# Optimization experiments

Measured on AMD Instinct MI355X. Metric: run time of the kernel, lower is better.

## Reference

```python
import jax, jax.numpy as jnp
import numpy as np

ALPHA = 0.1
EPS = 1e-10

def setup_inputs() -> dict:
    key = jax.random.key(0)
    k1, k2 = jax.random.split(key)
    x = jax.random.normal(k1, (64, 8192, 128), dtype=jnp.float32)   # [B, N, D]
    pv = jax.random.uniform(k2, (64, 128), dtype=jnp.float32)        # [M, D] prototypes (torch.rand init)
    return {"x": x, "pv": pv}

def _cdist(x, pv):
    # Euclidean pairwise distance via GEMM form: [B,N,D] x [M,D] -> [B,N,M]
    x2 = jnp.sum(x * x, axis=-1, keepdims=True)          # [B,N,1]
    p2 = jnp.sum(pv * pv, axis=-1)                        # [M]
    xp = jnp.einsum('bnd,md->bnm', x, pv)                 # [B,N,M]
    return jnp.sqrt(jnp.maximum(x2 + p2 - 2.0 * xp, 0.0))

def reference(x, pv):
    dist = _cdist(x, pv)                                  # [B,N,M]
    min_dist = jnp.min(dist, axis=1)                      # [B,M] closest patch per prototype
    min_pos = jnp.argmin(dist, axis=1)                    # [B,M]
    # pick, per batch, the patch position of the globally closest prototype (no-grad in original)
    idx = jnp.argmin(min_dist, axis=1)                    # [B]
    min_pos = min_pos[jnp.arange(min_pos.shape[0]), idx]  # [B]
    max_sim = jnp.exp(EPS - ALPHA * min_dist)             # [B,M]
    return (max_sim, min_pos)
```

## Files before the change

kernel.cpp:

```cpp
#include <hip/hip_runtime.h>
#include <cfloat>
#include <cmath>

#define B_ 64
#define N_ 8192
#define D_ 128
#define M_ 64
#define CROWS 64
#define NCHUNK 4
#define BROWS (CROWS*NCHUNK)
#define NBLK (N_/BROWS)
#define ALPHA_ 0.1f
#define EPS_ 1e-10f

typedef __attribute__((ext_vector_type(4))) float f32x4;
typedef __attribute__((ext_vector_type(8))) short bf16x8;
typedef __attribute__((ext_vector_type(4))) short s16x4;

__global__ __launch_bounds__(256, 3)
void protomin_mfma(const float* __restrict__ x, const float* __restrict__ pv,
                   float* __restrict__ wsv, int* __restrict__ wsa) {
    __shared__ short xhi[CROWS * D_];
    __shared__ short xlo[CROWS * D_];
    __shared__ float x2s[CROWS];
    __shared__ float redv[2][M_];
    __shared__ int   redp[2][M_];

    const int tid = threadIdx.x;
    const int w   = tid >> 6;
    const int l   = tid & 63;
    const int lm  = l & 15, lg = l >> 4;
    const int wr  = w & 1;
    const int wm  = w >> 1;
    const int bid = blockIdx.x;
    const int b   = bid >> 5;
    const int nbase = (bid & 31) * BROWS;

    const float* xblk = x + ((size_t)b * N_ + nbase) * D_;

    f32x4 nv[8];
    {
        const f32x4* src = (const f32x4*)xblk;
#pragma unroll
        for (int i = 0; i < 8; ++i) nv[i] = src[(w * 8 + i) * 64 + l];
    }

    bf16x8 Bh[2][4], Bl[2][4];
#pragma unroll
    for (int mti = 0; mti < 2; ++mti) {
#pragma unroll
        for (int kt = 0; kt < 4; ++kt) {
            const float* p = pv + (wm * 32 + mti * 16 + lm) * D_ + kt * 32 + lg * 8;
#pragma unroll
            for (int h = 0; h < 2; ++h) {
                f32x4 pq = *(const f32x4*)(p + 4 * h);
#pragma unroll
                for (int j = 0; j < 4; ++j) {
                    unsigned u = __float_as_uint(pq[j]);
                    float hf = __uint_as_float(u & 0xffff0000u);
                    Bh[mti][kt][4 * h + j] = (short)(u >> 16);
                    float rem = pq[j] - hf;
                    Bl[mti][kt][4 * h + j] = (short)(__float_as_uint(rem) >> 16);
                }
            }
        }
    }

    auto stage = [&]() {
#pragma unroll
        for (int i = 0; i < 8; ++i) {
            int seg = w * 8 + i;
            int row = seg * 2 + (l >> 5);
            int ks  = (l & 31) * 4;
            f32x4 v = nv[i];
            float s = v[0] * v[0];
            s = fmaf(v[1], v[1], s); s = fmaf(v[2], v[2], s); s = fmaf(v[3], v[3], s);
            s += __shfl_xor(s, 1);  s += __shfl_xor(s, 2);  s += __shfl_xor(s, 4);
            s += __shfl_xor(s, 8);  s += __shfl_xor(s, 16);
            if ((l & 31) == 0) x2s[row] = s;
            s16x4 hv, lv;
#pragma unroll
            for (int j = 0; j < 4; ++j) {
                unsigned u = __float_as_uint(v[j]);
                float hf = __uint_as_float(u & 0xffff0000u);
                hv[j] = (short)(u >> 16);
                float rem = v[j] - hf;
                lv[j] = (short)(__float_as_uint(rem) >> 16);
            }
            int sidx = row * D_ + (ks ^ ((row & 7) << 3));
            *(s16x4*)&xhi[sidx] = hv;
            *(s16x4*)&xlo[sidx] = lv;
        }
    };

    float bv[2]; int bp[2];
#pragma unroll
    for (int mti = 0; mti < 2; ++mti) { bv[mti] = FLT_MAX; bp[mti] = 0; }

    stage();
    __syncthreads();

    for (int c = 0; c < NCHUNK; ++c) {
        if (c + 1 < NCHUNK) {
            const f32x4* src = (const f32x4*)(xblk + (size_t)(c + 1) * CROWS * D_);
#pragma unroll
            for (int i = 0; i < 8; ++i) nv[i] = src[(w * 8 + i) * 64 + l];
        }

        f32x4 acc[2][2] = {};
#pragma unroll
        for (int kt = 0; kt < 4; ++kt) {
            bf16x8 ah[2], al[2];
#pragma unroll
            for (int rt = 0; rt < 2; ++rt) {
                int arow = wr * 32 + rt * 16 + lm;
                int koff = (kt * 32 + lg * 8) ^ ((arow & 7) << 3);
                ah[rt] = *(const bf16x8*)&xhi[arow * D_ + koff];
                al[rt] = *(const bf16x8*)&xlo[arow * D_ + koff];
            }
#pragma unroll
            for (int rt = 0; rt < 2; ++rt) {
#pragma unroll
                for (int mti = 0; mti < 2; ++mti) {
                    acc[rt][mti] = __builtin_amdgcn_mfma_f32_16x16x32_bf16(ah[rt], Bh[mti][kt], acc[rt][mti], 0, 0, 0);
                    acc[rt][mti] = __builtin_amdgcn_mfma_f32_16x16x32_bf16(al[rt], Bh[mti][kt], acc[rt][mti], 0, 0, 0);
                    acc[rt][mti] = __builtin_amdgcn_mfma_f32_16x16x32_bf16(ah[rt], Bl[mti][kt], acc[rt][mti], 0, 0, 0);
                }
            }
        }

#pragma unroll
        for (int rt = 0; rt < 2; ++rt) {
            const int rbase = wr * 32 + rt * 16 + lg * 4;
            float x2v[4];
#pragma unroll
            for (int r = 0; r < 4; ++r) x2v[r] = x2s[rbase + r];
            const int npos0 = nbase + c * CROWS + rbase;
#pragma unroll
            for (int mti = 0; mti < 2; ++mti) {
#pragma unroll
                for (int r = 0; r < 4; ++r) {
                    float cand = fmaf(-2.f, acc[rt][mti][r], x2v[r]);
                    if (cand < bv[mti]) { bv[mti] = cand; bp[mti] = npos0 + r; }
                }
            }
        }

        if (c + 1 < NCHUNK) {
            __syncthreads();
            stage();
            __syncthreads();
        }
    }

#pragma unroll
    for (int mti = 0; mti < 2; ++mti) {
        float v = bv[mti]; int p = bp[mti];
#pragma unroll
        for (int off = 16; off <= 32; off <<= 1) {
            float ov = __shfl_xor(v, off);
            int   op = __shfl_xor(p, off);
            if (ov < v || (ov == v && op < p)) { v = ov; p = op; }
        }
        if (l < 16) { redv[wr][wm * 32 + mti * 16 + l] = v;
                      redp[wr][wm * 32 + mti * 16 + l] = p; }
    }
    __syncthreads();

    if (tid < M_) {
        float v = redv[0][tid]; int p = redp[0][tid];
        float ov = redv[1][tid]; int op = redp[1][tid];
        if (ov < v || (ov == v && op < p)) { v = ov; p = op; }
        wsv[(size_t)bid * M_ + tid] = v;
        wsa[(size_t)bid * M_ + tid] = p;
    }
}

__global__ void finalize_kernel(const float* __restrict__ wsv,
                                const int* __restrict__ wsa,
                                const float* __restrict__ pv,
                                float* __restrict__ out) {
    const int b = blockIdx.x;
    const int m = threadIdx.x;

    float p2 = 0.f;
    const f32x4* pp = (const f32x4*)(pv + m * D_);
#pragma unroll 8
    for (int j = 0; j < 32; ++j) {
        f32x4 v = pp[j];
        p2 = fmaf(v[0], v[0], p2); p2 = fmaf(v[1], v[1], p2);
        p2 = fmaf(v[2], v[2], p2); p2 = fmaf(v[3], v[3], p2);
    }

    float v = FLT_MAX; int p = 0;
    for (int bc = 0; bc < NBLK; ++bc) {
        size_t idx = ((size_t)(b * NBLK + bc)) * M_ + m;
        float nv2 = wsv[idx]; int np = wsa[idx];
        if (nv2 < v || (nv2 == v && np < p)) { v = nv2; p = np; }
    }
    float dist = sqrtf(fmaxf(v + p2, 0.f));
    out[b * M_ + m] = expf(EPS_ - ALPHA_ * dist);

    __shared__ float sv[M_];
    __shared__ int   sa[M_];
    sv[m] = dist; sa[m] = p;
    __syncthreads();
    if (m == 0) {
        float best = FLT_MAX; int bpos = 0;
        for (int k = 0; k < M_; ++k)
            if (sv[k] < best) { best = sv[k]; bpos = sa[k]; }
        out[B_ * M_ + b] = (float)bpos;
    }
}

extern "C" void kernel_launch(void* const* d_in, const int* in_sizes, int n_in,
                              void* d_out, int out_size, void* d_ws, size_t ws_size,
                              hipStream_t stream) {
    const float* x  = (const float*)d_in[0];
    const float* pv = (const float*)d_in[1];
    float* out = (float*)d_out;

    float* wsv = (float*)d_ws;
    int*   wsa = (int*)((char*)d_ws + (size_t)B_ * NBLK * M_ * sizeof(float));

    hipLaunchKernelGGL(protomin_mfma, dim3(B_ * NBLK), dim3(256), 0, stream,
                       x, pv, wsv, wsa);
    hipLaunchKernelGGL(finalize_kernel, dim3(B_), dim3(M_), 0, stream,
                       wsv, wsa, pv, out);
}
```

Before: 378.5 us.

## Stream x tiles straight into a double-buffered LDS ring via global_load_lds

```diff
diff --git a/kernel.cpp b/kernel.cpp
--- a/kernel.cpp
+++ b/kernel.cpp
@@ -15,14 +15,15 @@
 
 typedef __attribute__((ext_vector_type(4))) float f32x4;
 typedef __attribute__((ext_vector_type(8))) short bf16x8;
-typedef __attribute__((ext_vector_type(4))) short s16x4;
-
-__global__ __launch_bounds__(256, 3)
+
+#define GLOAD_LDS16(gp, lp) __builtin_amdgcn_global_load_lds(              \
+    (const __attribute__((address_space(1))) void*)(gp),                   \
+    (__attribute__((address_space(3))) void*)(lp), 16, 0, 0)
+
+__global__ __launch_bounds__(256, 2)
 void protomin_mfma(const float* __restrict__ x, const float* __restrict__ pv,
                    float* __restrict__ wsv, int* __restrict__ wsa) {
-    __shared__ short xhi[CROWS * D_];
-    __shared__ short xlo[CROWS * D_];
-    __shared__ float x2s[CROWS];
+    __shared__ float ring[2][CROWS * D_];
     __shared__ float redv[2][M_];
     __shared__ int   redp[2][M_];
 
@@ -38,12 +39,16 @@
 
     const float* xblk = x + ((size_t)b * N_ + nbase) * D_;
 
-    f32x4 nv[8];
-    {
-        const f32x4* src = (const f32x4*)xblk;
-#pragma unroll
-        for (int i = 0; i < 8; ++i) nv[i] = src[(w * 8 + i) * 64 + l];
-    }
+    auto issue = [&](int buf, int c) {
+#pragma unroll
+        for (int i = 0; i < 8; ++i) {
+            int s    = w * 8 + i;
+            int row  = 2 * s + (l >> 5);
+            int gsl  = (l & 31) ^ (row & 7);
+            const float* gp = xblk + (size_t)c * CROWS * D_ + row * D_ + gsl * 4;
+            GLOAD_LDS16(gp, &ring[buf][s * 256]);
+        }
+    };
 
     bf16x8 Bh[2][4], Bl[2][4];
 #pragma unroll
@@ -66,57 +71,56 @@
         }
     }
 
-    auto stage = [&]() {
-#pragma unroll
-        for (int i = 0; i < 8; ++i) {
-            int seg = w * 8 + i;
-            int row = seg * 2 + (l >> 5);
-            int ks  = (l & 31) * 4;
-            f32x4 v = nv[i];
-            float s = v[0] * v[0];
-            s = fmaf(v[1], v[1], s); s = fmaf(v[2], v[2], s); s = fmaf(v[3], v[3], s);
-            s += __shfl_xor(s, 1);  s += __shfl_xor(s, 2);  s += __shfl_xor(s, 4);
-            s += __shfl_xor(s, 8);  s += __shfl_xor(s, 16);
-            if ((l & 31) == 0) x2s[row] = s;
-            s16x4 hv, lv;
-#pragma unroll
-            for (int j = 0; j < 4; ++j) {
-                unsigned u = __float_as_uint(v[j]);
-                float hf = __uint_as_float(u & 0xffff0000u);
-                hv[j] = (short)(u >> 16);
-                float rem = v[j] - hf;
-                lv[j] = (short)(__float_as_uint(rem) >> 16);
-            }
-            int sidx = row * D_ + (ks ^ ((row & 7) << 3));
-            *(s16x4*)&xhi[sidx] = hv;
-            *(s16x4*)&xlo[sidx] = lv;
-        }
-    };
-
     float bv[2]; int bp[2];
 #pragma unroll
     for (int mti = 0; mti < 2; ++mti) { bv[mti] = FLT_MAX; bp[mti] = 0; }
 
-    stage();
+    issue(0, 0);
+    issue(1, 1);
     __syncthreads();
 
+#pragma unroll
     for (int c = 0; c < NCHUNK; ++c) {
-        if (c + 1 < NCHUNK) {
-            const f32x4* src = (const f32x4*)(xblk + (size_t)(c + 1) * CROWS * D_);
-#pragma unroll
-            for (int i = 0; i < 8; ++i) nv[i] = src[(w * 8 + i) * 64 + l];
-        }
-
+        const int buf = c & 1;
         f32x4 acc[2][2] = {};
+        float x2p[2] = {0.f, 0.f};
+
 #pragma unroll
         for (int kt = 0; kt < 4; ++kt) {
             bf16x8 ah[2], al[2];
 #pragma unroll
             for (int rt = 0; rt < 2; ++rt) {
-                int arow = wr * 32 + rt * 16 + lm;
-                int koff = (kt * 32 + lg * 8) ^ ((arow & 7) << 3);
-                ah[rt] = *(const bf16x8*)&xhi[arow * D_ + koff];
-                al[rt] = *(const bf16x8*)&xlo[arow * D_ + koff];
+                const int row = wr * 32 + rt * 16 + lm;
+                const int rs  = row & 7;
+                const int j0  = kt * 8 + lg * 2;
+                const float* base = &ring[buf][row * D_];
+                f32x4 v0 = *(const f32x4*)(base + (((j0    ) ^ rs) << 2));
+                f32x4 v1 = *(const f32x4*)(base + (((j0 + 1) ^ rs) << 2));
+                x2p[rt] = fmaf(v0[0], v0[0], x2p[rt]);
+                x2p[rt] = fmaf(v0[1], v0[1], x2p[rt]);
+                x2p[rt] = fmaf(v0[2], v0[2], x2p[rt]);
+                x2p[rt] = fmaf(v0[3], v0[3], x2p[rt]);
+                x2p[rt] = fmaf(v1[0], v1[0], x2p[rt]);
+                x2p[rt] = fmaf(v1[1], v1[1], x2p[rt]);
+                x2p[rt] = fmaf(v1[2], v1[2], x2p[rt]);
+                x2p[rt] = fmaf(v1[3], v1[3], x2p[rt]);
+                union { bf16x8 v; unsigned u[4]; } AH, AL;
+#pragma unroll
+                for (int pq = 0; pq < 2; ++pq) {
+                    f32x4 vv = pq ? v1 : v0;
+#pragma unroll
+                    for (int e = 0; e < 2; ++e) {
+                        unsigned u0 = __float_as_uint(vv[2 * e]);
+                        unsigned u1 = __float_as_uint(vv[2 * e + 1]);
+                        unsigned h0 = u0 & 0xffff0000u, h1 = u1 & 0xffff0000u;
+                        AH.u[pq * 2 + e] = (u0 >> 16) | h1;
+                        float r0 = vv[2 * e]     - __uint_as_float(h0);
+                        float r1 = vv[2 * e + 1] - __uint_as_float(h1);
+                        AL.u[pq * 2 + e] = (__float_as_uint(r0) >> 16) |
+                                           (__float_as_uint(r1) & 0xffff0000u);
+                    }
+                }
+                ah[rt] = AH.v; al[rt] = AL.v;
             }
 #pragma unroll
             for (int rt = 0; rt < 2; ++rt) {
@@ -131,25 +135,28 @@
 
 #pragma unroll
         for (int rt = 0; rt < 2; ++rt) {
+            x2p[rt] += __shfl_xor(x2p[rt], 16);
+            x2p[rt] += __shfl_xor(x2p[rt], 32);
+        }
+
+#pragma unroll
+        for (int rt = 0; rt < 2; ++rt) {
             const int rbase = wr * 32 + rt * 16 + lg * 4;
-            float x2v[4];
-#pragma unroll
-            for (int r = 0; r < 4; ++r) x2v[r] = x2s[rbase + r];
             const int npos0 = nbase + c * CROWS + rbase;
 #pragma unroll
-            for (int mti = 0; mti < 2; ++mti) {
-#pragma unroll
-                for (int r = 0; r < 4; ++r) {
-                    float cand = fmaf(-2.f, acc[rt][mti][r], x2v[r]);
-                    if (cand < bv[mti]) { bv[mti] = cand; bp[mti] = npos0 + r; }
+            for (int q = 0; q < 4; ++q) {
+                float x2r = __shfl(x2p[rt], lg * 4 + q);
+#pragma unroll
+                for (int mti = 0; mti < 2; ++mti) {
+                    float cand = fmaf(-2.f, acc[rt][mti][q], x2r);
+                    if (cand < bv[mti]) { bv[mti] = cand; bp[mti] = npos0 + q; }
                 }
             }
         }
 
         if (c + 1 < NCHUNK) {
             __syncthreads();
-            stage();
-            __syncthreads();
+            if (c + 2 < NCHUNK) issue(buf, c + 2);
         }
     }
 
```

New measurement: 381.3 us. About the same (+0.7%).
